# Kernel tuning notes

Hardware: AMD Instinct MI355X
Metric: run time of the kernel (lower is better)

Reference implementation:

```python
import jax, jax.numpy as jnp
import numpy as np

K_SELECTED = 8  # config.num_selected_heads


def setup_inputs() -> dict:
    key = jax.random.key(0)
    k1, k2 = jax.random.split(key, 2)
    B, N, H, L = 4, 4096, 2048, 64
    x = jax.random.normal(k1, (B, N, H), dtype=jnp.float32)
    W_r = jax.random.normal(k2, (L, H), dtype=jnp.float32) * 0.02  # nn.Linear weight (L, H), no bias
    expert_bias = jnp.zeros((L,), dtype=jnp.float32)
    active_mask = jnp.ones((B, N), dtype=bool)
    return {"x": x, "W_r": W_r, "expert_bias": expert_bias, "active_mask": active_mask}


def reference(x, W_r, expert_bias, active_mask):
    L = expert_bias.shape[0]
    K = K_SELECTED
    # logits = x @ W_r.T  (bias-free routing projection)
    logits = jnp.einsum('bnh,lh->bnl', x, W_r)
    routing_scores = jax.nn.softmax(logits, axis=-1)            # unbiased probs
    biased_scores = jax.nn.softmax(logits + expert_bias, -1)    # biased probs for selection
    # top-K on biased scores -> selected head indices (B, N, K)
    _, selected_heads = jax.lax.top_k(biased_scores, K)
    # gather unbiased scores at selected indices and renormalize
    gathered = jnp.take_along_axis(routing_scores, selected_heads, axis=-1)
    routing_probs = gathered / gathered.sum(axis=-1, keepdims=True)
    # scatter into assignment mask: one-hot over L summed over K slots
    assignment_mask = jax.nn.one_hot(selected_heads, L, dtype=x.dtype).sum(axis=-2)  # (B, N, L)
    am = active_mask.astype(x.dtype)
    active_assignments = assignment_mask * am[..., None]
    num_active_assignments = am.sum() * K
    routing_freqs = active_assignments.sum(axis=(0, 1)) / num_active_assignments  # (L,)
    # LoadBalanceLoss.apply(expert_bias, routing_freqs): squared-imbalance value
    inv_L = 1.0 / L
    load_balance_loss = L * jnp.sum((routing_freqs - inv_L) ** 2)
    max_vio = jax.lax.stop_gradient(L * jnp.max(routing_freqs - inv_L))
    return selected_heads, routing_probs, load_balance_loss, max_vio
```

## Files before the change

kernel.cpp:

```cpp
#include <hip/hip_runtime.h>
#include <stdint.h>
#include <math.h>

constexpr int H     = 2048;
constexpr int L     = 64;
constexpr int K_SEL = 8;

constexpr int RPB   = 32;
constexpr int NCH   = 16;

constexpr float EPS_GAP = 1e-4f;

constexpr int WS_COUNTS = 0;
constexpr int WS_NFIX   = 128;
constexpr int WS_DONE   = 192;
constexpr int WS_LIST   = 256;
constexpr int WS_WT     = 16640;
constexpr int WS_WHC    = 147712;
constexpr int WS_WLC    = 213248;

typedef __attribute__((ext_vector_type(8))) short bf16x8;
typedef __attribute__((ext_vector_type(4))) float f32x4;

__device__ __forceinline__ void cvt_hi_lo(float c, short& h, short& l)
{
    unsigned u  = __float_as_uint(c);
    unsigned hb = (u + 0x7fffu + ((u >> 16) & 1u)) >> 16;
    float hf    = __uint_as_float(hb << 16);
    float lof   = c - hf;
    h = (short)hb;
    l = (short)(__float_as_uint(lof) >> 16);
}

__device__ __forceinline__ void cvt8(const float4& u0, const float4& u1,
                                     bf16x8& h, bf16x8& l)
{
    short hh, ll;
    cvt_hi_lo(u0.x, hh, ll); h[0] = hh; l[0] = ll;
    cvt_hi_lo(u0.y, hh, ll); h[1] = hh; l[1] = ll;
    cvt_hi_lo(u0.z, hh, ll); h[2] = hh; l[2] = ll;
    cvt_hi_lo(u0.w, hh, ll); h[3] = hh; l[3] = ll;
    cvt_hi_lo(u1.x, hh, ll); h[4] = hh; l[4] = ll;
    cvt_hi_lo(u1.y, hh, ll); h[5] = hh; l[5] = ll;
    cvt_hi_lo(u1.z, hh, ll); h[6] = hh; l[6] = ll;
    cvt_hi_lo(u1.w, hh, ll); h[7] = hh; l[7] = ll;
}

__device__ __forceinline__ f32x4 mm3(const bf16x8& ah, const bf16x8& al,
                                     const bf16x8& bh, const bf16x8& bl, f32x4 c)
{
    c = __builtin_amdgcn_mfma_f32_16x16x32_bf16(ah, bh, c, 0, 0, 0);
    c = __builtin_amdgcn_mfma_f32_16x16x32_bf16(ah, bl, c, 0, 0, 0);
    c = __builtin_amdgcn_mfma_f32_16x16x32_bf16(al, bh, c, 0, 0, 0);
    return c;
}

__global__ __launch_bounds__(256)
void prep(const float* __restrict__ Wr, float* __restrict__ Wt,
          unsigned int* __restrict__ wsu, short* __restrict__ whc,
          short* __restrict__ wlc)
{
    const int t = threadIdx.x, b = blockIdx.x;
    if (b == 32) {
        if (t < L + 1) wsu[WS_COUNTS + t] = 0u;
        if (t == 0)    wsu[WS_NFIX] = 0u;
        if (t == 1)    wsu[WS_DONE] = 0u;
        return;
    }
    if (b >= 33) {
        const int z = b - 33;
        const int e = 2 * z + (t >> 7);
        const int idx = t & 127;
        #pragma unroll
        for (int u = 0; u < 4; ++u) {
            const int f4i = idx + 128 * u;
            const int k   = 4 * f4i;
            const float4 v = ((const float4*)(Wr + (size_t)e * H))[f4i];
            short4 hh, ll;
            cvt_hi_lo(v.x, hh.x, ll.x);
            cvt_hi_lo(v.y, hh.y, ll.y);
            cvt_hi_lo(v.z, hh.z, ll.z);
            cvt_hi_lo(v.w, hh.w, ll.w);
            const int c  = k >> 5, kk = k & 31;
            const int di = (c * 64 + e) * 32 + kk;
            *(short4*)(whc + di) = hh;
            *(short4*)(wlc + di) = ll;
        }
        return;
    }
    __shared__ float tile[64 * 65];
    const int k0 = b * 64;
    {
        const int l = t >> 2, kq = (t & 3) * 16;
        #pragma unroll
        for (int j = 0; j < 4; ++j) {
            float4 v = *(const float4*)(Wr + (size_t)l * H + k0 + kq + 4 * j);
            int k = kq + 4 * j;
            tile[(k + 0) * 65 + l] = v.x;
            tile[(k + 1) * 65 + l] = v.y;
            tile[(k + 2) * 65 + l] = v.z;
            tile[(k + 3) * 65 + l] = v.w;
        }
    }
    __syncthreads();
    {
        const int k = t >> 2, lq = (t & 3) * 16;
        #pragma unroll
        for (int j = 0; j < 4; ++j) {
            int l2 = lq + 4 * j;
            float4 o = make_float4(tile[k * 65 + l2], tile[k * 65 + l2 + 1],
                                   tile[k * 65 + l2 + 2], tile[k * 65 + l2 + 3]);
            *(float4*)(Wt + (size_t)(k0 + k) * L + l2) = o;
        }
    }
}

__global__ __launch_bounds__(256, 2)
void router_mfma(const float* __restrict__ x, const short* __restrict__ whc,
                 const short* __restrict__ wlc, const float* __restrict__ bias,
                 const unsigned char* __restrict__ am,
                 float* __restrict__ out_sel, float* __restrict__ out_probs,
                 unsigned int* __restrict__ g_counts, unsigned int* __restrict__ nfix,
                 unsigned int* __restrict__ list)
{
    __shared__ __align__(16) float lg[4 * RPB * 68];
    __shared__ float bs[L];
    __shared__ unsigned int cnt[L + 1];

    const int t  = threadIdx.x;
    const int R0 = blockIdx.x * RPB;
    const int w  = t >> 6, l = t & 63;
    const int fr = l & 15;
    const int kg = l >> 4;
    const int kb = 8 * kg;

    if (t < L)     bs[t]  = bias[t];
    if (t < L + 1) cnt[t] = 0;

    f32x4 acc_00 = {}, acc_01 = {}, acc_02 = {}, acc_03 = {};
    f32x4 acc_10 = {}, acc_11 = {}, acc_12 = {}, acc_13 = {};

    const float* xp0 = x + (size_t)(R0 + fr) * H + kb;
    const float* xp1 = xp0 + (size_t)16 * H;
    const short* whp = whc + fr * 32 + kb;
    const short* wlp = wlc + fr * 32 + kb;

    #pragma unroll
    for (int ci = 0; ci < NCH; ++ci) {
        const int c  = NCH * w + ci;
        const int xo = 32 * c;
        const int wo = c * 2048;

        const float4 a00 = *(const float4*)(xp0 + xo);
        const float4 a01 = *(const float4*)(xp0 + xo + 4);
        const float4 a10 = *(const float4*)(xp1 + xo);
        const float4 a11 = *(const float4*)(xp1 + xo + 4);

        const bf16x8 bh0 = *(const bf16x8*)(whp + wo);
        const bf16x8 bh1 = *(const bf16x8*)(whp + wo + 512);
        const bf16x8 bh2 = *(const bf16x8*)(whp + wo + 1024);
        const bf16x8 bh3 = *(const bf16x8*)(whp + wo + 1536);
        const bf16x8 bl0 = *(const bf16x8*)(wlp + wo);
        const bf16x8 bl1 = *(const bf16x8*)(wlp + wo + 512);
        const bf16x8 bl2 = *(const bf16x8*)(wlp + wo + 1024);
        const bf16x8 bl3 = *(const bf16x8*)(wlp + wo + 1536);

        bf16x8 ah0, al0, ah1, al1;
        cvt8(a00, a01, ah0, al0);
        cvt8(a10, a11, ah1, al1);

        acc_00 = mm3(ah0, al0, bh0, bl0, acc_00);
        acc_01 = mm3(ah0, al0, bh1, bl1, acc_01);
        acc_02 = mm3(ah0, al0, bh2, bl2, acc_02);
        acc_03 = mm3(ah0, al0, bh3, bl3, acc_03);
        acc_10 = mm3(ah1, al1, bh0, bl0, acc_10);
        acc_11 = mm3(ah1, al1, bh1, bl1, acc_11);
        acc_12 = mm3(ah1, al1, bh2, bl2, acc_12);
        acc_13 = mm3(ah1, al1, bh3, bl3, acc_13);
    }

    {
        float* lgw = lg + w * (RPB * 68);
        const int rb = 4 * kg;
        #pragma unroll
        for (int r = 0; r < 4; ++r) {
            lgw[(rb + r)      * 68 + fr     ] = acc_00[r];
            lgw[(rb + r)      * 68 + fr + 16] = acc_01[r];
            lgw[(rb + r)      * 68 + fr + 32] = acc_02[r];
            lgw[(rb + r)      * 68 + fr + 48] = acc_03[r];
            lgw[(rb + r + 16) * 68 + fr     ] = acc_10[r];
            lgw[(rb + r + 16) * 68 + fr + 16] = acc_11[r];
            lgw[(rb + r + 16) * 68 + fr + 32] = acc_12[r];
            lgw[(rb + r + 16) * 68 + fr + 48] = acc_13[r];
        }
    }
    __syncthreads();

    #pragma unroll
    for (int q = 0; q < 9; ++q) {
        const int p = t + 256 * q;
        if (p < RPB * 68)
            lg[p] = (lg[p] + lg[RPB * 68 + p]) + (lg[2 * RPB * 68 + p] + lg[3 * RPB * 68 + p]);
    }
    __syncthreads();

    {
        const int tj   = t & 7;
        const int lrow = t >> 3;
        const int grow = R0 + lrow;

        float rv[8], lv[8];
        {
            const float* lp = &lg[lrow * 68 + 8 * tj];
            const float4 v0 = *(const float4*)(lp);
            const float4 v1 = *(const float4*)(lp + 4);
            rv[0] = v0.x; rv[1] = v0.y; rv[2] = v0.z; rv[3] = v0.w;
            rv[4] = v1.x; rv[5] = v1.y; rv[6] = v1.z; rv[7] = v1.w;
            #pragma unroll
            for (int i = 0; i < 8; ++i) lv[i] = rv[i] + bs[8 * tj + i];
        }

        unsigned msk = 0;
        int   selidx[K_SEL];
        float selraw[K_SEL];
        float prev = 0.f, gmin = INFINITY;

        #pragma unroll
        for (int kk = 0; kk < K_SEL + 1; ++kk) {
            float best = -INFINITY; int bi = 1 << 30; float braw = 0.f;
            #pragma unroll
            for (int i = 0; i < 8; ++i) {
                const bool free_ = !((msk >> i) & 1u);
                if (free_ && lv[i] > best) { best = lv[i]; bi = 8 * tj + i; braw = rv[i]; }
            }
            #pragma unroll
            for (int off = 1; off <= 4; off <<= 1) {
                const float ov  = __shfl_xor(best, off);
                const int   oi  = __shfl_xor(bi,   off);
                const float orw = __shfl_xor(braw, off);
                if (ov > best || (ov == best && oi < bi)) { best = ov; bi = oi; braw = orw; }
            }
            if (kk > 0) gmin = fminf(gmin, prev - best);
            prev = best;
            if (kk < K_SEL) {
                if ((bi >> 3) == tj) msk |= 1u << (bi & 7);
                selidx[kk] = bi;
                selraw[kk] = braw;
            }
        }

        if (gmin < EPS_GAP) {
            if (tj == 0) {
                unsigned int pp = atomicAdd(nfix, 1u);
                list[pp] = (unsigned int)grow;
            }
        } else {
            float mx = -INFINITY;
            #pragma unroll
            for (int kk = 0; kk < K_SEL; ++kk) mx = fmaxf(mx, selraw[kk]);
            float e[K_SEL], ssum = 0.f;
            #pragma unroll
            for (int kk = 0; kk < K_SEL; ++kk) { e[kk] = expf(selraw[kk] - mx); ssum += e[kk]; }
            float myp = 0.f; int myi = 0;
            #pragma unroll
            for (int kk = 0; kk < K_SEL; ++kk)
                if (kk == tj) { myp = e[kk] / ssum; myi = selidx[kk]; }
            out_sel  [(size_t)grow * K_SEL + tj] = (float)myi;
            out_probs[(size_t)grow * K_SEL + tj] = myp;
            if (am[grow]) {
                atomicAdd(&cnt[myi], 1u);
                if (tj == 0) atomicAdd(&cnt[L], 1u);
            }
        }
    }
    __syncthreads();
    if (t < L + 1 && cnt[t]) atomicAdd(&g_counts[t], cnt[t]);
}

__global__ __launch_bounds__(256)
void fixup_fin(const float* __restrict__ x, const float* __restrict__ Wt,
               const float* __restrict__ bias, const unsigned char* __restrict__ am,
               const unsigned int* __restrict__ nfix, const unsigned int* __restrict__ list,
               float* __restrict__ out_sel, float* __restrict__ out_probs,
               unsigned int* __restrict__ g_counts, unsigned int* __restrict__ done,
               float* __restrict__ out_scalars)
{
    const int lane = threadIdx.x & 63;
    const int wid  = (blockIdx.x << 2) | (threadIdx.x >> 6);
    const int nw   = gridDim.x << 2;
    const int n    = (int)*nfix;
    const double bl = (double)bias[lane];

    for (int i = wid; i < n; i += nw) {
        const int row = (int)list[i];
        const float* xr = x + (size_t)row * H;
        double a0 = 0.0, a1 = 0.0, a2 = 0.0, a3 = 0.0;
        #pragma unroll 2
        for (int k = 0; k < H; k += 16) {
            float4 x0 = *(const float4*)(xr + k);
            float4 x1 = *(const float4*)(xr + k + 4);
            float4 x2 = *(const float4*)(xr + k + 8);
            float4 x3 = *(const float4*)(xr + k + 12);
            a0 = fma((double)x0.x, (double)Wt[(k +  0) * L + lane], a0);
            a1 = fma((double)x0.y, (double)Wt[(k +  1) * L + lane], a1);
            a2 = fma((double)x0.z, (double)Wt[(k +  2) * L + lane], a2);
            a3 = fma((double)x0.w, (double)Wt[(k +  3) * L + lane], a3);
            a0 = fma((double)x1.x, (double)Wt[(k +  4) * L + lane], a0);
            a1 = fma((double)x1.y, (double)Wt[(k +  5) * L + lane], a1);
            a2 = fma((double)x1.z, (double)Wt[(k +  6) * L + lane], a2);
            a3 = fma((double)x1.w, (double)Wt[(k +  7) * L + lane], a3);
            a0 = fma((double)x2.x, (double)Wt[(k +  8) * L + lane], a0);
            a1 = fma((double)x2.y, (double)Wt[(k +  9) * L + lane], a1);
            a2 = fma((double)x2.z, (double)Wt[(k + 10) * L + lane], a2);
            a3 = fma((double)x2.w, (double)Wt[(k + 11) * L + lane], a3);
            a0 = fma((double)x3.x, (double)Wt[(k + 12) * L + lane], a0);
            a1 = fma((double)x3.y, (double)Wt[(k + 13) * L + lane], a1);
            a2 = fma((double)x3.z, (double)Wt[(k + 14) * L + lane], a2);
            a3 = fma((double)x3.w, (double)Wt[(k + 15) * L + lane], a3);
        }
        double acc = (a0 + a1) + (a2 + a3);

        double v = acc + bl;
        int    widx[K_SEL];
        double wlog[K_SEL];
        #pragma unroll
        for (int kk = 0; kk < K_SEL; ++kk) {
            double mv = v; int mi = lane;
            #pragma unroll
            for (int off = 32; off; off >>= 1) {
                double ov = __shfl_xor(mv, off);
                int    oi = __shfl_xor(mi, off);
                if (ov > mv || (ov == mv && oi < mi)) { mv = ov; mi = oi; }
            }
            widx[kk] = mi;
            wlog[kk] = __shfl(acc, mi);
            if (lane == mi) v = -INFINITY;
        }

        double mx = -INFINITY;
        #pragma unroll
        for (int kk = 0; kk < K_SEL; ++kk) mx = fmax(mx, wlog[kk]);
        float e[K_SEL], ssum = 0.f;
        #pragma unroll
        for (int kk = 0; kk < K_SEL; ++kk) { e[kk] = expf((float)(wlog[kk] - mx)); ssum += e[kk]; }

        if (lane < K_SEL) {
            out_sel[(size_t)row * K_SEL + lane]   = (float)widx[lane];
            out_probs[(size_t)row * K_SEL + lane] = e[lane] / ssum;
        }
        if (am[row]) {
            if (lane < K_SEL)  atomicAdd(&g_counts[widx[lane]], 1u);
            if (lane == K_SEL) atomicAdd(&g_counts[L], 1u);
        }
    }

    __shared__ bool last;
    __syncthreads();
    if (threadIdx.x == 0) {
        __threadfence();
        last = (atomicAdd(done, 1u) == (unsigned)gridDim.x - 1u);
    }
    __syncthreads();
    if (!last) return;

    const int l = threadIdx.x;
    if (l < L) {
        const unsigned cl = atomicAdd(&g_counts[l], 0u);
        const unsigned ct = atomicAdd(&g_counts[L], 0u);
        const float denom = (float)ct * (float)K_SEL;
        const float f = (float)cl / denom;
        float d  = f - 1.0f / (float)L;
        float sq = d * d;
        #pragma unroll
        for (int o = 32; o > 0; o >>= 1) {
            sq += __shfl_down(sq, o);
            d = fmaxf(d, __shfl_down(d, o));
        }
        if (l == 0) {
            out_scalars[0] = (float)L * sq;
            out_scalars[1] = (float)L * d;
        }
    }
}

extern "C" void kernel_launch(void* const* d_in, const int* in_sizes, int n_in,
                              void* d_out, int out_size, void* d_ws, size_t ws_size,
                              hipStream_t stream)
{
    const float* x          = (const float*)d_in[0];
    const float* Wr         = (const float*)d_in[1];
    const float* bias       = (const float*)d_in[2];
    const unsigned char* am = (const unsigned char*)d_in[3];
    float* out = (float*)d_out;
    float* wsf = (float*)d_ws;
    unsigned int* wsu = (unsigned int*)d_ws;

    const int rows = in_sizes[3];

    float* out_sel   = out;
    float* out_probs = out + (size_t)rows * K_SEL;
    float* out_scal  = out + (size_t)rows * K_SEL * 2;

    short* whc = (short*)(wsu + WS_WHC);
    short* wlc = (short*)(wsu + WS_WLC);

    hipLaunchKernelGGL(prep,        dim3(65),         dim3(256), 0, stream,
                       Wr, wsf + WS_WT, wsu, whc, wlc);
    hipLaunchKernelGGL(router_mfma, dim3(rows / RPB), dim3(256), 0, stream,
                       x, whc, wlc, bias, am, out_sel, out_probs,
                       wsu + WS_COUNTS, wsu + WS_NFIX, wsu + WS_LIST);
    hipLaunchKernelGGL(fixup_fin,   dim3(256),        dim3(256), 0, stream,
                       x, wsf + WS_WT, bias, am, wsu + WS_NFIX, wsu + WS_LIST,
                       out_sel, out_probs, wsu + WS_COUNTS, wsu + WS_DONE,
                       out_scal);
}
```

Baseline: 270.9 us.

## Halve router rows per block, raise occupancy, double-buffer MFMA operand loads

Rows per block drop from 32 to 16, so each wave keeps four accumulators instead of eight and the grid has twice as many blocks. The launch-bounds occupancy hint rises from 2 to 4 blocks per CU. The K loop now prefetches the next chunk's x and weight fragments into a second register set while the current chunk is converted and fed to the MFMAs, to hide global-load latency. In exchange, the bf16 weight fragments are re-read twice as often per row, and only half the threads take part in the per-row top-k epilogue.

```diff
diff --git a/kernel.cpp b/kernel.cpp
--- a/kernel.cpp
+++ b/kernel.cpp
@@ -6,7 +6,7 @@
 constexpr int L     = 64;
 constexpr int K_SEL = 8;
 
-constexpr int RPB   = 32;
+constexpr int RPB   = 16;
 constexpr int NCH   = 16;
 
 constexpr float EPS_GAP = 1e-4f;
@@ -53,6 +53,39 @@
     c = __builtin_amdgcn_mfma_f32_16x16x32_bf16(ah, bl, c, 0, 0, 0);
     c = __builtin_amdgcn_mfma_f32_16x16x32_bf16(al, bh, c, 0, 0, 0);
     return c;
+}
+
+struct Frag {
+    float4 a0, a1;
+    bf16x8 bh0, bh1, bh2, bh3, bl0, bl1, bl2, bl3;
+};
+
+__device__ __forceinline__ void load_frag(Frag& f, const float* xp0,
+                                          const short* whp, const short* wlp,
+                                          int c)
+{
+    const int xo = 32 * c, wo = 2048 * c;
+    f.a0  = *(const float4*)(xp0 + xo);
+    f.a1  = *(const float4*)(xp0 + xo + 4);
+    f.bh0 = *(const bf16x8*)(whp + wo);
+    f.bh1 = *(const bf16x8*)(whp + wo + 512);
+    f.bh2 = *(const bf16x8*)(whp + wo + 1024);
+    f.bh3 = *(const bf16x8*)(whp + wo + 1536);
+    f.bl0 = *(const bf16x8*)(wlp + wo);
+    f.bl1 = *(const bf16x8*)(wlp + wo + 512);
+    f.bl2 = *(const bf16x8*)(wlp + wo + 1024);
+    f.bl3 = *(const bf16x8*)(wlp + wo + 1536);
+}
+
+__device__ __forceinline__ void consume(const Frag& f, f32x4& c0, f32x4& c1,
+                                        f32x4& c2, f32x4& c3)
+{
+    bf16x8 ah, al;
+    cvt8(f.a0, f.a1, ah, al);
+    c0 = mm3(ah, al, f.bh0, f.bl0, c0);
+    c1 = mm3(ah, al, f.bh1, f.bl1, c1);
+    c2 = mm3(ah, al, f.bh2, f.bl2, c2);
+    c3 = mm3(ah, al, f.bh3, f.bl3, c3);
 }
 
 __global__ __launch_bounds__(256)
@@ -115,7 +148,7 @@
     }
 }
 
-__global__ __launch_bounds__(256, 2)
+__global__ __launch_bounds__(256, 4)
 void router_mfma(const float* __restrict__ x, const short* __restrict__ whc,
                  const short* __restrict__ wlc, const float* __restrict__ bias,
                  const unsigned char* __restrict__ am,
@@ -137,46 +170,23 @@
     if (t < L)     bs[t]  = bias[t];
     if (t < L + 1) cnt[t] = 0;
 
-    f32x4 acc_00 = {}, acc_01 = {}, acc_02 = {}, acc_03 = {};
-    f32x4 acc_10 = {}, acc_11 = {}, acc_12 = {}, acc_13 = {};
+    f32x4 acc0 = {}, acc1 = {}, acc2 = {}, acc3 = {};
 
     const float* xp0 = x + (size_t)(R0 + fr) * H + kb;
-    const float* xp1 = xp0 + (size_t)16 * H;
     const short* whp = whc + fr * 32 + kb;
     const short* wlp = wlc + fr * 32 + kb;
 
-    #pragma unroll
-    for (int ci = 0; ci < NCH; ++ci) {
-        const int c  = NCH * w + ci;
-        const int xo = 32 * c;
-        const int wo = c * 2048;
-
-        const float4 a00 = *(const float4*)(xp0 + xo);
-        const float4 a01 = *(const float4*)(xp0 + xo + 4);
-        const float4 a10 = *(const float4*)(xp1 + xo);
-        const float4 a11 = *(const float4*)(xp1 + xo + 4);
-
-        const bf16x8 bh0 = *(const bf16x8*)(whp + wo);
-        const bf16x8 bh1 = *(const bf16x8*)(whp + wo + 512);
-        const bf16x8 bh2 = *(const bf16x8*)(whp + wo + 1024);
-        const bf16x8 bh3 = *(const bf16x8*)(whp + wo + 1536);
-        const bf16x8 bl0 = *(const bf16x8*)(wlp + wo);
-        const bf16x8 bl1 = *(const bf16x8*)(wlp + wo + 512);
-        const bf16x8 bl2 = *(const bf16x8*)(wlp + wo + 1024);
-        const bf16x8 bl3 = *(const bf16x8*)(wlp + wo + 1536);
-
-        bf16x8 ah0, al0, ah1, al1;
-        cvt8(a00, a01, ah0, al0);
-        cvt8(a10, a11, ah1, al1);
-
-        acc_00 = mm3(ah0, al0, bh0, bl0, acc_00);
-        acc_01 = mm3(ah0, al0, bh1, bl1, acc_01);
-        acc_02 = mm3(ah0, al0, bh2, bl2, acc_02);
-        acc_03 = mm3(ah0, al0, bh3, bl3, acc_03);
-        acc_10 = mm3(ah1, al1, bh0, bl0, acc_10);
-        acc_11 = mm3(ah1, al1, bh1, bl1, acc_11);
-        acc_12 = mm3(ah1, al1, bh2, bl2, acc_12);
-        acc_13 = mm3(ah1, al1, bh3, bl3, acc_13);
+    {
+        const int c0 = NCH * w;
+        Frag fA, fB;
+        load_frag(fA, xp0, whp, wlp, c0);
+        #pragma unroll
+        for (int ci = 0; ci < NCH; ci += 2) {
+            load_frag(fB, xp0, whp, wlp, c0 + ci + 1);
+            consume(fA, acc0, acc1, acc2, acc3);
+            if (ci + 2 < NCH) load_frag(fA, xp0, whp, wlp, c0 + ci + 2);
+            consume(fB, acc0, acc1, acc2, acc3);
+        }
     }
 
     {
@@ -184,27 +194,23 @@
         const int rb = 4 * kg;
         #pragma unroll
         for (int r = 0; r < 4; ++r) {
-            lgw[(rb + r)      * 68 + fr     ] = acc_00[r];
-            lgw[(rb + r)      * 68 + fr + 16] = acc_01[r];
-            lgw[(rb + r)      * 68 + fr + 32] = acc_02[r];
-            lgw[(rb + r)      * 68 + fr + 48] = acc_03[r];
-            lgw[(rb + r + 16) * 68 + fr     ] = acc_10[r];
-            lgw[(rb + r + 16) * 68 + fr + 16] = acc_11[r];
-            lgw[(rb + r + 16) * 68 + fr + 32] = acc_12[r];
-            lgw[(rb + r + 16) * 68 + fr + 48] = acc_13[r];
+            lgw[(rb + r) * 68 + fr     ] = acc0[r];
+            lgw[(rb + r) * 68 + fr + 16] = acc1[r];
+            lgw[(rb + r) * 68 + fr + 32] = acc2[r];
+            lgw[(rb + r) * 68 + fr + 48] = acc3[r];
         }
     }
     __syncthreads();
 
     #pragma unroll
-    for (int q = 0; q < 9; ++q) {
+    for (int q = 0; q < 5; ++q) {
         const int p = t + 256 * q;
         if (p < RPB * 68)
             lg[p] = (lg[p] + lg[RPB * 68 + p]) + (lg[2 * RPB * 68 + p] + lg[3 * RPB * 68 + p]);
     }
     __syncthreads();
 
-    {
+    if (t < 8 * RPB) {
         const int tj   = t & 7;
         const int lrow = t >> 3;
         const int grow = R0 + lrow;
```

Measured after the change: 287.5 us. +6.1%, slower.

## Stage x tiles through LDS with async double-buffered loads, split waves by output column

Applied to the files above, without the earlier changes.

Replaces the per-wave K-split, where each wave read x straight from global memory and the four partial logit tiles were reduced in LDS, with a column split: each wave owns 16 of the 64 experts across the full K range. x rows are staged into LDS in 256-wide chunks using global_load_lds in a double buffer, so the next chunk loads while the current one is consumed, and weight fragments are software-prefetched one step ahead. This removes the cross-wave LDS reduction and cuts the number of accumulator registers. In exchange every wave reads the whole x tile from LDS and the convert to bf16 hi/lo is repeated four times across waves, with a barrier per stage.

```diff
diff --git a/kernel.cpp b/kernel.cpp
--- a/kernel.cpp
+++ b/kernel.cpp
@@ -7,7 +7,9 @@
 constexpr int K_SEL = 8;
 
 constexpr int RPB   = 32;
-constexpr int NCH   = 16;
+constexpr int BK    = 256;
+constexpr int NSTG  = H / BK;
+constexpr int XROW  = 260;
 
 constexpr float EPS_GAP = 1e-4f;
 
@@ -21,6 +23,13 @@
 
 typedef __attribute__((ext_vector_type(8))) short bf16x8;
 typedef __attribute__((ext_vector_type(4))) float f32x4;
+
+__device__ __forceinline__ void gld16(const float* g, float* l)
+{
+    __builtin_amdgcn_global_load_lds(
+        (const __attribute__((address_space(1))) unsigned int*)g,
+        (__attribute__((address_space(3))) unsigned int*)l, 16, 0, 0);
+}
 
 __device__ __forceinline__ void cvt_hi_lo(float c, short& h, short& l)
 {
@@ -123,84 +132,75 @@
                  unsigned int* __restrict__ g_counts, unsigned int* __restrict__ nfix,
                  unsigned int* __restrict__ list)
 {
-    __shared__ __align__(16) float lg[4 * RPB * 68];
+    __shared__ __align__(16) float xs[2][RPB * XROW];
+    __shared__ __align__(16) float lg[RPB * 68];
     __shared__ float bs[L];
     __shared__ unsigned int cnt[L + 1];
 
-    const int t  = threadIdx.x;
-    const int R0 = blockIdx.x * RPB;
-    const int w  = t >> 6, l = t & 63;
-    const int fr = l & 15;
-    const int kg = l >> 4;
-    const int kb = 8 * kg;
+    const int t    = threadIdx.x;
+    const int R0   = blockIdx.x * RPB;
+    const int w    = t >> 6;
+    const int lane = t & 63;
+    const int fr   = lane & 15;
+    const int kg   = lane >> 4;
+    const int kb   = 8 * kg;
 
     if (t < L)     bs[t]  = bias[t];
     if (t < L + 1) cnt[t] = 0;
 
-    f32x4 acc_00 = {}, acc_01 = {}, acc_02 = {}, acc_03 = {};
-    f32x4 acc_10 = {}, acc_11 = {}, acc_12 = {}, acc_13 = {};
-
-    const float* xp0 = x + (size_t)(R0 + fr) * H + kb;
-    const float* xp1 = xp0 + (size_t)16 * H;
-    const short* whp = whc + fr * 32 + kb;
-    const short* wlp = wlc + fr * 32 + kb;
+    f32x4 acc0 = {}, acc1 = {};
+
+    const short* whp = whc + w * 512 + fr * 32 + kb;
+    const short* wlp = wlc + w * 512 + fr * 32 + kb;
 
     #pragma unroll
-    for (int ci = 0; ci < NCH; ++ci) {
-        const int c  = NCH * w + ci;
-        const int xo = 32 * c;
-        const int wo = c * 2048;
-
-        const float4 a00 = *(const float4*)(xp0 + xo);
-        const float4 a01 = *(const float4*)(xp0 + xo + 4);
-        const float4 a10 = *(const float4*)(xp1 + xo);
-        const float4 a11 = *(const float4*)(xp1 + xo + 4);
-
-        const bf16x8 bh0 = *(const bf16x8*)(whp + wo);
-        const bf16x8 bh1 = *(const bf16x8*)(whp + wo + 512);
-        const bf16x8 bh2 = *(const bf16x8*)(whp + wo + 1024);
-        const bf16x8 bh3 = *(const bf16x8*)(whp + wo + 1536);
-        const bf16x8 bl0 = *(const bf16x8*)(wlp + wo);
-        const bf16x8 bl1 = *(const bf16x8*)(wlp + wo + 512);
-        const bf16x8 bl2 = *(const bf16x8*)(wlp + wo + 1024);
-        const bf16x8 bl3 = *(const bf16x8*)(wlp + wo + 1536);
-
-        bf16x8 ah0, al0, ah1, al1;
-        cvt8(a00, a01, ah0, al0);
-        cvt8(a10, a11, ah1, al1);
-
-        acc_00 = mm3(ah0, al0, bh0, bl0, acc_00);
-        acc_01 = mm3(ah0, al0, bh1, bl1, acc_01);
-        acc_02 = mm3(ah0, al0, bh2, bl2, acc_02);
-        acc_03 = mm3(ah0, al0, bh3, bl3, acc_03);
-        acc_10 = mm3(ah1, al1, bh0, bl0, acc_10);
-        acc_11 = mm3(ah1, al1, bh1, bl1, acc_11);
-        acc_12 = mm3(ah1, al1, bh2, bl2, acc_12);
-        acc_13 = mm3(ah1, al1, bh3, bl3, acc_13);
-    }
-
-    {
-        float* lgw = lg + w * (RPB * 68);
-        const int rb = 4 * kg;
-        #pragma unroll
-        for (int r = 0; r < 4; ++r) {
-            lgw[(rb + r)      * 68 + fr     ] = acc_00[r];
-            lgw[(rb + r)      * 68 + fr + 16] = acc_01[r];
-            lgw[(rb + r)      * 68 + fr + 32] = acc_02[r];
-            lgw[(rb + r)      * 68 + fr + 48] = acc_03[r];
-            lgw[(rb + r + 16) * 68 + fr     ] = acc_10[r];
-            lgw[(rb + r + 16) * 68 + fr + 16] = acc_11[r];
-            lgw[(rb + r + 16) * 68 + fr + 32] = acc_12[r];
-            lgw[(rb + r + 16) * 68 + fr + 48] = acc_13[r];
-        }
-    }
-    __syncthreads();
+    for (int j = 0; j < 8; ++j) {
+        const int r = 8 * w + j;
+        gld16(x + (size_t)(R0 + r) * H + 4 * lane, &xs[0][r * XROW]);
+    }
+    bf16x8 wh_c = *(const bf16x8*)(whp);
+    bf16x8 wl_c = *(const bf16x8*)(wlp);
+    __syncthreads();
+
+    for (int s = 0; s < NSTG; ++s) {
+        const int p = s & 1;
+        if (s + 1 < NSTG) {
+            const int k0n = BK * (s + 1);
+            #pragma unroll
+            for (int j = 0; j < 8; ++j) {
+                const int r = 8 * w + j;
+                gld16(x + (size_t)(R0 + r) * H + k0n + 4 * lane,
+                      &xs[p ^ 1][r * XROW]);
+            }
+        }
+        #pragma unroll
+        for (int kc = 0; kc < 8; ++kc) {
+            const int c = 8 * s + kc;
+            bf16x8 wh_n = wh_c, wl_n = wl_c;
+            if (c + 1 < 64) {
+                wh_n = *(const bf16x8*)(whp + 2048 * (c + 1));
+                wl_n = *(const bf16x8*)(wlp + 2048 * (c + 1));
+            }
+            const float* x0 = &xs[p][fr * XROW + 32 * kc + kb];
+            const float* x1 = &xs[p][(fr + 16) * XROW + 32 * kc + kb];
+            const float4 a00 = *(const float4*)(x0);
+            const float4 a01 = *(const float4*)(x0 + 4);
+            const float4 a10 = *(const float4*)(x1);
+            const float4 a11 = *(const float4*)(x1 + 4);
+            bf16x8 ah0, al0, ah1, al1;
+            cvt8(a00, a01, ah0, al0);
+            cvt8(a10, a11, ah1, al1);
+            acc0 = mm3(ah0, al0, wh_c, wl_c, acc0);
+            acc1 = mm3(ah1, al1, wh_c, wl_c, acc1);
+            wh_c = wh_n; wl_c = wl_n;
+        }
+        __syncthreads();
+    }
 
     #pragma unroll
-    for (int q = 0; q < 9; ++q) {
-        const int p = t + 256 * q;
-        if (p < RPB * 68)
-            lg[p] = (lg[p] + lg[RPB * 68 + p]) + (lg[2 * RPB * 68 + p] + lg[3 * RPB * 68 + p]);
+    for (int r = 0; r < 4; ++r) {
+        lg[(4 * kg + r)      * 68 + 16 * w + fr] = acc0[r];
+        lg[(4 * kg + r + 16) * 68 + 16 * w + fr] = acc1[r];
     }
     __syncthreads();
 
```

New measurement: 273.7 us. Within noise of the previous version (+1.0%).
